# Optimization experiments

Measured on AMD Instinct MI355X. Metric: run time of the kernel, lower is better.

Reference implementation:

```python
import jax, jax.numpy as jnp
import numpy as np

N = 100_000   # num nodes
E = 1_600_000 # num edges (before self-loops)
IN = 128      # in_channels (FEATURE_DIM)
H = 64        # hidden_channels (HIDDEN_DIM)
NEG_SLOPE = 0.2


def setup_inputs() -> dict:
    key = jax.random.key(0)
    ks = jax.random.split(key, 8)
    s = 0.05
    return {
        "x": jax.random.normal(ks[0], (N, IN), jnp.float32),
        "edge_index": jax.random.randint(ks[1], (2, E), 0, N, jnp.int32),
        "W_gat": jax.random.normal(ks[2], (IN, H), jnp.float32) * s,
        "att_src": jax.random.normal(ks[3], (H,), jnp.float32) * s,
        "att_dst": jax.random.normal(ks[4], (H,), jnp.float32) * s,
        "b_gat": jnp.zeros((H,), jnp.float32),
        "W1": jax.random.normal(ks[5], (H, H), jnp.float32) * s,
        "b1": jnp.zeros((H,), jnp.float32),
        "W2": jax.random.normal(ks[6], (H, H), jnp.float32) * s,
        "b2": jnp.zeros((H,), jnp.float32),
    }


def _add_self_loops(src, dst, n):
    loop = jnp.arange(n, dtype=src.dtype)
    return jnp.concatenate([src, loop]), jnp.concatenate([dst, loop])


def _segment_softmax(e, seg, n):
    # numerically stable softmax over edges grouped by target node
    m = jax.ops.segment_max(e, seg, num_segments=n)
    m = jnp.where(jnp.isfinite(m), m, 0.0)  # empty segments
    ex = jnp.exp(e - m[seg])
    s = jax.ops.segment_sum(ex, seg, num_segments=n)
    return ex / (s[seg] + 1e-16)


def gat_conv(x, W, a_src, a_dst, b, src, dst, n):
    # PyG GATConv, heads=1: h = xW; e_ij = LeakyReLU(a_s.h_j + a_d.h_i)
    h = x @ W                                   # [N,H]
    alpha_s = h @ a_src                         # [N]
    alpha_d = h @ a_dst                         # [N]
    e = jax.nn.leaky_relu(alpha_s[src] + alpha_d[dst], NEG_SLOPE)  # [E]
    alpha = _segment_softmax(e, dst, n)         # [E]
    out = jax.ops.segment_sum(alpha[:, None] * h[src], dst, num_segments=n)
    return out + b


def gcn_conv(x, W, b, src, dst, n):
    # PyG GCNConv: symmetric normalization D^-1/2 A D^-1/2 (self-loops already added)
    h = x @ W                                   # [N,H]
    deg = jax.ops.segment_sum(jnp.ones(src.shape, h.dtype), dst, num_segments=n)
    dinv = jnp.where(deg > 0, jax.lax.rsqrt(deg), 0.0)
    norm = dinv[src] * dinv[dst]                # [E]
    out = jax.ops.segment_sum(norm[:, None] * h[src], dst, num_segments=n)
    return out + b


def reference(x, edge_index, W_gat, att_src, att_dst, b_gat, W1, b1, W2, b2):
    n = x.shape[0]
    src, dst = _add_self_loops(edge_index[0], edge_index[1], n)
    h = jax.nn.relu(gat_conv(x, W_gat, att_src, att_dst, b_gat, src, dst, n))
    h = jax.nn.relu(gcn_conv(h, W1, b1, src, dst, n))
    h = gcn_conv(h, W2, b2, src, dst, n)
    return h
```

## Files before the change

### kernel.cpp

```cpp
#include <hip/hip_runtime.h>
#include <hip/hip_bf16.h>
#include <math.h>

#define IN_CH 128
#define H_CH  64
#define PBLK  256
#define PTHR  512
#define BKT   256
#define MAXBK 400


__device__ inline float bflo(unsigned u) { return __uint_as_float(u << 16); }
__device__ inline float bfhi(unsigned u) { return __uint_as_float(u & 0xffff0000u); }
__device__ inline unsigned short f2bf(float f) {
    unsigned x = __float_as_uint(f);
    return (unsigned short)((x + 0x7fffu + ((x >> 16) & 1u)) >> 16);
}


__global__ __launch_bounds__(PTHR) void passA(const int* __restrict__ ei, int E, int n,
                                              int nbk, int* __restrict__ blkhist) {
    __shared__ int hist[MAXBK];
    int tot = E + n;
    int CH = (tot + gridDim.x - 1) / gridDim.x;
    int beg = blockIdx.x * CH, end = min(tot, beg + CH);
    for (int k = threadIdx.x; k < nbk; k += blockDim.x) hist[k] = 0;
    __syncthreads();
    for (int idx = beg + threadIdx.x; idx < end; idx += blockDim.x) {
        int d = (idx < E) ? ei[E + idx] : (idx - E);
        atomicAdd(&hist[d >> 8], 1);
    }
    __syncthreads();
    for (int k = threadIdx.x; k < nbk; k += blockDim.x)
        blkhist[(size_t)blockIdx.x * nbk + k] = hist[k];
}

__global__ __launch_bounds__(PBLK) void passB1(const int* __restrict__ blkhist,
                                               int* __restrict__ blkbase,
                                               int* __restrict__ btot, int nbk) {
    __shared__ int sh[PBLK];
    int k = blockIdx.x, t = threadIdx.x;
    int v = blkhist[(size_t)t * nbk + k];
    sh[t] = v;
    __syncthreads();
    for (int off = 1; off < PBLK; off <<= 1) {
        int x = (t >= off) ? sh[t - off] : 0;
        __syncthreads();
        sh[t] += x;
        __syncthreads();
    }
    blkbase[(size_t)t * nbk + k] = sh[t] - v;
    if (t == PBLK - 1) btot[k] = sh[PBLK - 1];
}

__global__ __launch_bounds__(512) void passB2(const int* __restrict__ btot,
                                              int* __restrict__ bbase, int nbk, int tot) {
    __shared__ int sh[512];
    int t = threadIdx.x;
    int v = (t < nbk) ? btot[t] : 0;
    sh[t] = v;
    __syncthreads();
    for (int off = 1; off < 512; off <<= 1) {
        int x = (t >= off) ? sh[t - off] : 0;
        __syncthreads();
        sh[t] += x;
        __syncthreads();
    }
    if (t < nbk) bbase[t] = sh[t] - v;
    if (t == 0) bbase[nbk] = tot;
}

__global__ __launch_bounds__(PTHR) void passC(const int* __restrict__ ei, int E, int n, int nbk,
                                              const int* __restrict__ bbase,
                                              const int* __restrict__ blkbase,
                                              int2* __restrict__ pairs) {
    __shared__ int cur[MAXBK];
    int tot = E + n;
    int CH = (tot + gridDim.x - 1) / gridDim.x;
    int beg = blockIdx.x * CH, end = min(tot, beg + CH);
    for (int k = threadIdx.x; k < nbk; k += blockDim.x)
        cur[k] = bbase[k] + blkbase[(size_t)blockIdx.x * nbk + k];
    __syncthreads();
    for (int idx = beg + threadIdx.x; idx < end; idx += blockDim.x) {
        int s, d;
        if (idx < E) { s = ei[idx]; d = ei[E + idx]; }
        else         { s = idx - E; d = idx - E; }
        int pos = atomicAdd(&cur[d >> 8], 1);
        pairs[pos] = make_int2(s, d);
    }
}

__global__ __launch_bounds__(BKT) void passD(const int2* __restrict__ pairs,
                                             const int* __restrict__ bbase, int n, int nbk, int EP,
                                             int* __restrict__ esrc, int* __restrict__ offsets,
                                             float* __restrict__ dinv) {
    __shared__ int cnt[BKT];
    __shared__ int sh[BKT];
    __shared__ int cur[BKT];
    int k = blockIdx.x;
    int nbeg = k << 8;
    int t = threadIdx.x;
    int ebeg = bbase[k], eend = bbase[k + 1];
    cnt[t] = 0;
    __syncthreads();
    for (int e = ebeg + t; e < eend; e += BKT) {
        int2 p = pairs[e];
        atomicAdd(&cnt[p.y - nbeg], 1);
    }
    __syncthreads();
    int v = cnt[t];
    sh[t] = v;
    __syncthreads();
    for (int off = 1; off < BKT; off <<= 1) {
        int x = (t >= off) ? sh[t - off] : 0;
        __syncthreads();
        sh[t] += x;
        __syncthreads();
    }
    int lp = sh[t] - v;
    cur[t] = lp;
    int gn = nbeg + t;
    if (gn < n) {
        offsets[gn] = ebeg + lp;
        dinv[gn] = rsqrtf((float)v);
    }
    __syncthreads();
    for (int e = ebeg + t; e < eend; e += BKT) {
        int2 p = pairs[e];
        int pos = ebeg + atomicAdd(&cur[p.y - nbeg], 1);
        esrc[pos] = p.x;
    }
    if (k == 0 && t == 0) offsets[n] = EP;
}


template <int K, bool GAT, bool OUTBF, bool BIASF>
__global__ __launch_bounds__(512, 6) void gemm_tiled(const float* __restrict__ X,
                                                     const float* __restrict__ W,
                                                     void* __restrict__ outv,
                                                     const float* __restrict__ asw,
                                                     const float* __restrict__ adw,
                                                     float* __restrict__ alpha_s,
                                                     float* __restrict__ alpha_d,
                                                     const float* __restrict__ bias, int n) {
    __shared__ float Wl[K][68];
    int t  = threadIdx.x;
    int tx = t & 15, ty = t >> 4;
    int r0 = blockIdx.x * 128;

#pragma unroll
    for (int i = 0; i < K / 32; i++) {
        int f = t + 512 * i;
        int k = f >> 4, cq = (f & 15) << 2;
        float4 v = *(const float4*)(W + k * H_CH + cq);
        *(float4*)&Wl[k][cq] = v;
    }
    __syncthreads();

    const float* xp[4];
#pragma unroll
    for (int j = 0; j < 4; j++) {
        int r = r0 + 4 * ty + j;
        xp[j] = X + (size_t)(r < n ? r : 0) * K;
    }

    float acc[4][4] = {};
#pragma unroll 4
    for (int k4 = 0; k4 < K; k4 += 4) {
        float4 xr[4], wr[4];
#pragma unroll
        for (int j = 0; j < 4; j++)  xr[j]  = *(const float4*)(xp[j] + k4);
#pragma unroll
        for (int kk = 0; kk < 4; kk++) wr[kk] = *(const float4*)&Wl[k4 + kk][4 * tx];
#pragma unroll
        for (int j = 0; j < 4; j++) {
            acc[j][0] += xr[j].x * wr[0].x; acc[j][1] += xr[j].x * wr[0].y;
            acc[j][2] += xr[j].x * wr[0].z; acc[j][3] += xr[j].x * wr[0].w;
            acc[j][0] += xr[j].y * wr[1].x; acc[j][1] += xr[j].y * wr[1].y;
            acc[j][2] += xr[j].y * wr[1].z; acc[j][3] += xr[j].y * wr[1].w;
            acc[j][0] += xr[j].z * wr[2].x; acc[j][1] += xr[j].z * wr[2].y;
            acc[j][2] += xr[j].z * wr[2].z; acc[j][3] += xr[j].z * wr[2].w;
            acc[j][0] += xr[j].w * wr[3].x; acc[j][1] += xr[j].w * wr[3].y;
            acc[j][2] += xr[j].w * wr[3].z; acc[j][3] += xr[j].w * wr[3].w;
        }
    }

    float4 bvv = make_float4(0.f, 0.f, 0.f, 0.f);
    if (BIASF) bvv = *(const float4*)(bias + 4 * tx);

#pragma unroll
    for (int j = 0; j < 4; j++) {
        int r = r0 + 4 * ty + j;
        if (r < n) {
            float o0 = acc[j][0] + bvv.x, o1 = acc[j][1] + bvv.y;
            float o2 = acc[j][2] + bvv.z, o3 = acc[j][3] + bvv.w;
            if (OUTBF) {
                ushort4 o;
                o.x = f2bf(o0); o.y = f2bf(o1); o.z = f2bf(o2); o.w = f2bf(o3);
                *(ushort4*)((unsigned short*)outv + (size_t)r * H_CH + 4 * tx) = o;
            } else {
                *(float4*)((float*)outv + (size_t)r * H_CH + 4 * tx) =
                    make_float4(o0, o1, o2, o3);
            }
        }
    }

    if (GAT) {
        float va0 = asw[4 * tx], va1 = asw[4 * tx + 1], va2 = asw[4 * tx + 2], va3 = asw[4 * tx + 3];
        float vd0 = adw[4 * tx], vd1 = adw[4 * tx + 1], vd2 = adw[4 * tx + 2], vd3 = adw[4 * tx + 3];
#pragma unroll
        for (int j = 0; j < 4; j++) {
            float s1 = acc[j][0] * va0 + acc[j][1] * va1 + acc[j][2] * va2 + acc[j][3] * va3;
            float s2 = acc[j][0] * vd0 + acc[j][1] * vd1 + acc[j][2] * vd2 + acc[j][3] * vd3;
#pragma unroll
            for (int off = 8; off; off >>= 1) {
                s1 += __shfl_xor(s1, off, 16);
                s2 += __shfl_xor(s2, off, 16);
            }
            int r = r0 + 4 * ty + j;
            if (tx == 0 && r < n) { alpha_s[r] = s1; alpha_d[r] = s2; }
        }
    }
}


__global__ __launch_bounds__(256) void gat_gather(const unsigned short* __restrict__ h,
                                                  const int* __restrict__ offs,
                                                  const int* __restrict__ esrc,
                                                  const float* __restrict__ as,
                                                  const float* __restrict__ ad,
                                                  const float* __restrict__ bias,
                                                  float* __restrict__ out, int n) {
    __shared__ int2 sh[4][64];
    int lane = threadIdx.x & 63;
    int wid  = threadIdx.x >> 6;
    int q = lane >> 4, c = lane & 15;
    int gw = (blockIdx.x * blockDim.x + threadIdx.x) >> 6;
    int nw = (gridDim.x * blockDim.x) >> 6;
    float4 bv = *(const float4*)(bias + 4 * c);
    for (int i = gw; i < n; i += nw) {
        int beg = offs[i], end = offs[i + 1];
        float adi = ad[i];
        float a0 = 0.f, a1 = 0.f, a2 = 0.f, a3 = 0.f, s = 0.f;
        for (int base = beg; base < end; base += 64) {
            int l = base + lane;
            int sj = 0; float p = 0.f;
            if (l < end) {
                sj = esrc[l];
                float a = as[sj] + adi;
                float ev = a > 0.f ? a : 0.2f * a;
                p = __expf(ev);
            }
            sh[wid][lane] = make_int2(sj, __float_as_int(p));
            int cnt = min(64, end - base);
            int k = 0;
            for (; k + 8 <= cnt; k += 8) {
                int2 tA = sh[wid][k + q];
                int2 tB = sh[wid][k + 4 + q];
                float pA = __int_as_float(tA.y);
                float pB = __int_as_float(tB.y);
                uint2 uA = *(const uint2*)(h + (size_t)tA.x * H_CH + 4 * c);
                uint2 uB = *(const uint2*)(h + (size_t)tB.x * H_CH + 4 * c);
                a0 += pA * bflo(uA.x); a1 += pA * bfhi(uA.x);
                a2 += pA * bflo(uA.y); a3 += pA * bfhi(uA.y);
                a0 += pB * bflo(uB.x); a1 += pB * bfhi(uB.x);
                a2 += pB * bflo(uB.y); a3 += pB * bfhi(uB.y);
                s += pA + pB;
            }
            for (; k < cnt; k += 4) {
                int2 tA = sh[wid][k + q];
                float pA = __int_as_float(tA.y);
                uint2 uA = *(const uint2*)(h + (size_t)tA.x * H_CH + 4 * c);
                a0 += pA * bflo(uA.x); a1 += pA * bfhi(uA.x);
                a2 += pA * bflo(uA.y); a3 += pA * bfhi(uA.y);
                s += pA;
            }
        }
        a0 += __shfl_xor(a0, 16, 64); a0 += __shfl_xor(a0, 32, 64);
        a1 += __shfl_xor(a1, 16, 64); a1 += __shfl_xor(a1, 32, 64);
        a2 += __shfl_xor(a2, 16, 64); a2 += __shfl_xor(a2, 32, 64);
        a3 += __shfl_xor(a3, 16, 64); a3 += __shfl_xor(a3, 32, 64);
        s  += __shfl_xor(s, 16, 64);  s  += __shfl_xor(s, 32, 64);
        float invs = 1.f / (s + 1e-16f);
        if (q == 0) {
            float4 o;
            o.x = fmaxf(a0 * invs + bv.x, 0.f);
            o.y = fmaxf(a1 * invs + bv.y, 0.f);
            o.z = fmaxf(a2 * invs + bv.z, 0.f);
            o.w = fmaxf(a3 * invs + bv.w, 0.f);
            *(float4*)(out + (size_t)i * H_CH + 4 * c) = o;
        }
    }
}


template <bool OUTBF, bool RELU, bool BIASF>
__global__ __launch_bounds__(256) void gcn_gather(const unsigned short* __restrict__ h,
                                                  const int* __restrict__ offs,
                                                  const int* __restrict__ esrc,
                                                  const float* __restrict__ dinv,
                                                  const float* __restrict__ bias,
                                                  void* __restrict__ outv, int n) {
    __shared__ int2 sh[4][64];
    int lane = threadIdx.x & 63;
    int wid  = threadIdx.x >> 6;
    int q = lane >> 4, c = lane & 15;
    int gw = (blockIdx.x * blockDim.x + threadIdx.x) >> 6;
    int nw = (gridDim.x * blockDim.x) >> 6;
    float4 bv = make_float4(0.f, 0.f, 0.f, 0.f);
    if (BIASF) bv = *(const float4*)(bias + 4 * c);
    for (int i = gw; i < n; i += nw) {
        int beg = offs[i], end = offs[i + 1];
        float a0 = 0.f, a1 = 0.f, a2 = 0.f, a3 = 0.f;
        for (int base = beg; base < end; base += 64) {
            int l = base + lane;
            int sj = 0; float wl = 0.f;
            if (l < end) { sj = esrc[l]; wl = dinv[sj]; }
            sh[wid][lane] = make_int2(sj, __float_as_int(wl));
            int cnt = min(64, end - base);
            int k = 0;
            for (; k + 8 <= cnt; k += 8) {
                int2 tA = sh[wid][k + q];
                int2 tB = sh[wid][k + 4 + q];
                float pA = __int_as_float(tA.y);
                float pB = __int_as_float(tB.y);
                uint2 uA = *(const uint2*)(h + (size_t)tA.x * H_CH + 4 * c);
                uint2 uB = *(const uint2*)(h + (size_t)tB.x * H_CH + 4 * c);
                a0 += pA * bflo(uA.x); a1 += pA * bfhi(uA.x);
                a2 += pA * bflo(uA.y); a3 += pA * bfhi(uA.y);
                a0 += pB * bflo(uB.x); a1 += pB * bfhi(uB.x);
                a2 += pB * bflo(uB.y); a3 += pB * bfhi(uB.y);
            }
            for (; k < cnt; k += 4) {
                int2 tA = sh[wid][k + q];
                float pA = __int_as_float(tA.y);
                uint2 uA = *(const uint2*)(h + (size_t)tA.x * H_CH + 4 * c);
                a0 += pA * bflo(uA.x); a1 += pA * bfhi(uA.x);
                a2 += pA * bflo(uA.y); a3 += pA * bfhi(uA.y);
            }
        }
        a0 += __shfl_xor(a0, 16, 64); a0 += __shfl_xor(a0, 32, 64);
        a1 += __shfl_xor(a1, 16, 64); a1 += __shfl_xor(a1, 32, 64);
        a2 += __shfl_xor(a2, 16, 64); a2 += __shfl_xor(a2, 32, 64);
        a3 += __shfl_xor(a3, 16, 64); a3 += __shfl_xor(a3, 32, 64);
        float di = dinv[i];
        if (q == 0) {
            float v0 = a0 * di + bv.x, v1 = a1 * di + bv.y;
            float v2 = a2 * di + bv.z, v3 = a3 * di + bv.w;
            if (RELU) {
                v0 = fmaxf(v0, 0.f); v1 = fmaxf(v1, 0.f);
                v2 = fmaxf(v2, 0.f); v3 = fmaxf(v3, 0.f);
            }
            if (OUTBF) {
                ushort4 o;
                o.x = f2bf(v0); o.y = f2bf(v1); o.z = f2bf(v2); o.w = f2bf(v3);
                *(ushort4*)((unsigned short*)outv + (size_t)i * H_CH + 4 * c) = o;
            } else {
                *(float4*)((float*)outv + (size_t)i * H_CH + 4 * c) =
                    make_float4(v0, v1, v2, v3);
            }
        }
    }
}


extern "C" void kernel_launch(void* const* d_in, const int* in_sizes, int n_in,
                              void* d_out, int out_size, void* d_ws, size_t ws_size,
                              hipStream_t stream) {
    const float* x       = (const float*)d_in[0];
    const int*   ei      = (const int*)d_in[1];
    const float* W_gat   = (const float*)d_in[2];
    const float* att_src = (const float*)d_in[3];
    const float* att_dst = (const float*)d_in[4];
    const float* b_gat   = (const float*)d_in[5];
    const float* W1      = (const float*)d_in[6];
    const float* b1      = (const float*)d_in[7];
    const float* W2      = (const float*)d_in[8];
    const float* b2      = (const float*)d_in[9];
    float* out = (float*)d_out;

    const int N  = in_sizes[0] / IN_CH;
    const int E  = in_sizes[1] / 2;
    const int EP = E + N;
    const int NBK = (N + BKT - 1) / BKT;
    const int NT  = (N + 127) / 128;

    char* p = (char*)d_ws;
    auto alloc = [&](size_t bytes) -> void* {
        void* r = (void*)p;
        p += (bytes + 255) & ~(size_t)255;
        return r;
    };
    float* bufA    = (float*)alloc((size_t)N * H_CH * 4);
    unsigned short* hbf  = (unsigned short*)alloc((size_t)N * H_CH * 2);
    unsigned short* hbf2 = (unsigned short*)alloc((size_t)N * H_CH * 2);
    float* alpha_s = (float*)alloc((size_t)N * 4);
    float* alpha_d = (float*)alloc((size_t)N * 4);
    float* dinv    = (float*)alloc((size_t)N * 4);
    int*   offsets = (int*)alloc((size_t)(N + 1) * 4);
    int*   esrc    = (int*)alloc((size_t)EP * 4);
    int2*  pairs   = (int2*)alloc((size_t)EP * 8);
    int*   blkhist = (int*)alloc((size_t)PBLK * NBK * 4);
    int*   blkbase = (int*)alloc((size_t)PBLK * NBK * 4);
    int*   btot    = (int*)alloc((size_t)(NBK + 1) * 4);
    int*   bbase   = (int*)alloc((size_t)(NBK + 1) * 4);

    passA<<<PBLK, PTHR, 0, stream>>>(ei, E, N, NBK, blkhist);
    passB1<<<NBK, PBLK, 0, stream>>>(blkhist, blkbase, btot, NBK);
    passB2<<<1, 512, 0, stream>>>(btot, bbase, NBK, EP);
    passC<<<PBLK, PTHR, 0, stream>>>(ei, E, N, NBK, bbase, blkbase, pairs);
    passD<<<NBK, BKT, 0, stream>>>(pairs, bbase, N, NBK, EP, esrc, offsets, dinv);

    gemm_tiled<IN_CH, true, true, false><<<NT, 512, 0, stream>>>(x, W_gat, hbf, att_src, att_dst,
                                                                 alpha_s, alpha_d, nullptr, N);
    gat_gather<<<2048, 256, 0, stream>>>(hbf, offsets, esrc, alpha_s, alpha_d, b_gat, bufA, N);

    gemm_tiled<H_CH, false, true, false><<<NT, 512, 0, stream>>>(bufA, W1, hbf, nullptr, nullptr,
                                                                 nullptr, nullptr, nullptr, N);
    gcn_gather<true, true, true><<<2048, 256, 0, stream>>>(hbf, offsets, esrc, dinv, b1, hbf2, N);

    gcn_gather<false, false, false><<<2048, 256, 0, stream>>>(hbf2, offsets, esrc, dinv, nullptr,
                                                              bufA, N);
    gemm_tiled<H_CH, false, false, true><<<NT, 512, 0, stream>>>(bufA, W2, out, nullptr, nullptr,
                                                                 nullptr, nullptr, b2, N);
}
```

Before: 251.3 us.

## Replace FP32 tiled GEMMs with bf16 MFMA GEMM and fold attention into weights

The three dense projections now run as a wave-level bf16 MFMA kernel (16x16x32) with W fragments kept in registers, instead of an FP32 FMA tile kernel. GAT attention logits are computed straight from x using the precomputed vectors W·att_src and W·att_dst, which a small prep kernel produces. This is meant to cut GEMM compute time, but the inputs are rounded to bf16 before the MFMA and outputs are written with scalar, less coalesced stores. The GEMMs are a minor part of a pipeline that is dominated by the gathers.

```diff
diff --git a/kernel.cpp b/kernel.cpp
--- a/kernel.cpp
+++ b/kernel.cpp
@@ -9,12 +9,25 @@
 #define BKT   256
 #define MAXBK 400
 
+typedef __attribute__((ext_vector_type(8))) short bf16x8;
+typedef __attribute__((ext_vector_type(4))) float f32x4;
+
 
 __device__ inline float bflo(unsigned u) { return __uint_as_float(u << 16); }
 __device__ inline float bfhi(unsigned u) { return __uint_as_float(u & 0xffff0000u); }
 __device__ inline unsigned short f2bf(float f) {
     unsigned x = __float_as_uint(f);
     return (unsigned short)((x + 0x7fffu + ((x >> 16) & 1u)) >> 16);
+}
+__device__ inline bf16x8 pack8(float4 lo, float4 hi) {
+    union { bf16x8 v; unsigned short u[8]; } r;
+    r.u[0] = f2bf(lo.x); r.u[1] = f2bf(lo.y); r.u[2] = f2bf(lo.z); r.u[3] = f2bf(lo.w);
+    r.u[4] = f2bf(hi.x); r.u[5] = f2bf(hi.y); r.u[6] = f2bf(hi.z); r.u[7] = f2bf(hi.w);
+    return r.v;
+}
+__device__ inline float dot8(float4 a0, float4 a1, float4 b0, float4 b1) {
+    return a0.x * b0.x + a0.y * b0.y + a0.z * b0.z + a0.w * b0.w
+         + a1.x * b1.x + a1.y * b1.y + a1.z * b1.z + a1.w * b1.w;
 }
 
 
@@ -134,91 +147,108 @@
 }
 
 
+__global__ void wprep(const float* __restrict__ W, const float* __restrict__ as,
+                      const float* __restrict__ ad, float* __restrict__ w_as,
+                      float* __restrict__ w_ad, int K) {
+    int k = blockIdx.x * blockDim.x + threadIdx.x;
+    if (k < K) {
+        float s = 0.f, d = 0.f;
+        for (int c = 0; c < H_CH; c++) {
+            float w = W[(size_t)k * H_CH + c];
+            s += w * as[c];
+            d += w * ad[c];
+        }
+        w_as[k] = s;
+        w_ad[k] = d;
+    }
+}
+
+
 template <int K, bool GAT, bool OUTBF, bool BIASF>
-__global__ __launch_bounds__(512, 6) void gemm_tiled(const float* __restrict__ X,
-                                                     const float* __restrict__ W,
-                                                     void* __restrict__ outv,
-                                                     const float* __restrict__ asw,
-                                                     const float* __restrict__ adw,
-                                                     float* __restrict__ alpha_s,
-                                                     float* __restrict__ alpha_d,
-                                                     const float* __restrict__ bias, int n) {
-    __shared__ float Wl[K][68];
-    int t  = threadIdx.x;
-    int tx = t & 15, ty = t >> 4;
-    int r0 = blockIdx.x * 128;
-
-#pragma unroll
-    for (int i = 0; i < K / 32; i++) {
-        int f = t + 512 * i;
-        int k = f >> 4, cq = (f & 15) << 2;
-        float4 v = *(const float4*)(W + k * H_CH + cq);
-        *(float4*)&Wl[k][cq] = v;
-    }
-    __syncthreads();
-
-    const float* xp[4];
-#pragma unroll
-    for (int j = 0; j < 4; j++) {
-        int r = r0 + 4 * ty + j;
-        xp[j] = X + (size_t)(r < n ? r : 0) * K;
-    }
-
-    float acc[4][4] = {};
-#pragma unroll 4
-    for (int k4 = 0; k4 < K; k4 += 4) {
-        float4 xr[4], wr[4];
-#pragma unroll
-        for (int j = 0; j < 4; j++)  xr[j]  = *(const float4*)(xp[j] + k4);
-#pragma unroll
-        for (int kk = 0; kk < 4; kk++) wr[kk] = *(const float4*)&Wl[k4 + kk][4 * tx];
-#pragma unroll
-        for (int j = 0; j < 4; j++) {
-            acc[j][0] += xr[j].x * wr[0].x; acc[j][1] += xr[j].x * wr[0].y;
-            acc[j][2] += xr[j].x * wr[0].z; acc[j][3] += xr[j].x * wr[0].w;
-            acc[j][0] += xr[j].y * wr[1].x; acc[j][1] += xr[j].y * wr[1].y;
-            acc[j][2] += xr[j].y * wr[1].z; acc[j][3] += xr[j].y * wr[1].w;
-            acc[j][0] += xr[j].z * wr[2].x; acc[j][1] += xr[j].z * wr[2].y;
-            acc[j][2] += xr[j].z * wr[2].z; acc[j][3] += xr[j].z * wr[2].w;
-            acc[j][0] += xr[j].w * wr[3].x; acc[j][1] += xr[j].w * wr[3].y;
-            acc[j][2] += xr[j].w * wr[3].z; acc[j][3] += xr[j].w * wr[3].w;
-        }
-    }
-
-    float4 bvv = make_float4(0.f, 0.f, 0.f, 0.f);
-    if (BIASF) bvv = *(const float4*)(bias + 4 * tx);
-
-#pragma unroll
-    for (int j = 0; j < 4; j++) {
-        int r = r0 + 4 * ty + j;
-        if (r < n) {
-            float o0 = acc[j][0] + bvv.x, o1 = acc[j][1] + bvv.y;
-            float o2 = acc[j][2] + bvv.z, o3 = acc[j][3] + bvv.w;
-            if (OUTBF) {
-                ushort4 o;
-                o.x = f2bf(o0); o.y = f2bf(o1); o.z = f2bf(o2); o.w = f2bf(o3);
-                *(ushort4*)((unsigned short*)outv + (size_t)r * H_CH + 4 * tx) = o;
-            } else {
-                *(float4*)((float*)outv + (size_t)r * H_CH + 4 * tx) =
-                    make_float4(o0, o1, o2, o3);
-            }
-        }
-    }
-
-    if (GAT) {
-        float va0 = asw[4 * tx], va1 = asw[4 * tx + 1], va2 = asw[4 * tx + 2], va3 = asw[4 * tx + 3];
-        float vd0 = adw[4 * tx], vd1 = adw[4 * tx + 1], vd2 = adw[4 * tx + 2], vd3 = adw[4 * tx + 3];
-#pragma unroll
-        for (int j = 0; j < 4; j++) {
-            float s1 = acc[j][0] * va0 + acc[j][1] * va1 + acc[j][2] * va2 + acc[j][3] * va3;
-            float s2 = acc[j][0] * vd0 + acc[j][1] * vd1 + acc[j][2] * vd2 + acc[j][3] * vd3;
-#pragma unroll
-            for (int off = 8; off; off >>= 1) {
-                s1 += __shfl_xor(s1, off, 16);
-                s2 += __shfl_xor(s2, off, 16);
-            }
-            int r = r0 + 4 * ty + j;
-            if (tx == 0 && r < n) { alpha_s[r] = s1; alpha_d[r] = s2; }
+__global__ __launch_bounds__(256) void mfma_gemm(const float* __restrict__ X,
+                                                 const float* __restrict__ W,
+                                                 void* __restrict__ outv,
+                                                 const float* __restrict__ w_as,
+                                                 const float* __restrict__ w_ad,
+                                                 float* __restrict__ alpha_s,
+                                                 float* __restrict__ alpha_d,
+                                                 const float* __restrict__ bias, int n) {
+    constexpr int KF = K / 32;
+    int lane = threadIdx.x & 63;
+    int wid  = threadIdx.x >> 6;
+    int col  = lane & 15;
+    int grp  = lane >> 4;
+
+    bf16x8 bfr[KF][4];
+#pragma unroll
+    for (int kf = 0; kf < KF; kf++) {
+        int kb = 32 * kf + 8 * grp;
+#pragma unroll
+        for (int cf = 0; cf < 4; cf++) {
+            float w0[8];
+#pragma unroll
+            for (int e = 0; e < 8; e++)
+                w0[e] = W[(size_t)(kb + e) * H_CH + 16 * cf + col];
+            bfr[kf][cf] = pack8(make_float4(w0[0], w0[1], w0[2], w0[3]),
+                                make_float4(w0[4], w0[5], w0[6], w0[7]));
+        }
+    }
+    float bb[4] = {0.f, 0.f, 0.f, 0.f};
+    if (BIASF) {
+#pragma unroll
+        for (int cf = 0; cf < 4; cf++) bb[cf] = bias[16 * cf + col];
+    }
+
+    int gw = blockIdx.x * (blockDim.x >> 6) + wid;
+    int nw = gridDim.x * (blockDim.x >> 6);
+    int ns = (n + 15) >> 4;
+    for (int s = gw; s < ns; s += nw) {
+        int r0 = s << 4;
+        int r  = r0 + col;
+        const float* xr = X + (size_t)(r < n ? r : 0) * K;
+        bf16x8 afr[KF];
+        float ps = 0.f, pd = 0.f;
+#pragma unroll
+        for (int kf = 0; kf < KF; kf++) {
+            int kb = 32 * kf + 8 * grp;
+            float4 x0 = *(const float4*)(xr + kb);
+            float4 x1 = *(const float4*)(xr + kb + 4);
+            if (GAT) {
+                float4 s0 = *(const float4*)(w_as + kb);
+                float4 s1 = *(const float4*)(w_as + kb + 4);
+                float4 d0 = *(const float4*)(w_ad + kb);
+                float4 d1 = *(const float4*)(w_ad + kb + 4);
+                ps += dot8(x0, x1, s0, s1);
+                pd += dot8(x0, x1, d0, d1);
+            }
+            afr[kf] = pack8(x0, x1);
+        }
+        f32x4 acc[4];
+#pragma unroll
+        for (int cf = 0; cf < 4; cf++) {
+            acc[cf] = (f32x4){0.f, 0.f, 0.f, 0.f};
+#pragma unroll
+            for (int kf = 0; kf < KF; kf++)
+                acc[cf] = __builtin_amdgcn_mfma_f32_16x16x32_bf16(afr[kf], bfr[kf][cf],
+                                                                  acc[cf], 0, 0, 0);
+        }
+#pragma unroll
+        for (int cf = 0; cf < 4; cf++) {
+            int cc = 16 * cf + col;
+#pragma unroll
+            for (int g = 0; g < 4; g++) {
+                int rr = r0 + 4 * grp + g;
+                if (rr < n) {
+                    float v = acc[cf][g] + bb[cf];
+                    if (OUTBF) ((unsigned short*)outv)[(size_t)rr * H_CH + cc] = f2bf(v);
+                    else       ((float*)outv)[(size_t)rr * H_CH + cc] = v;
+                }
+            }
+        }
+        if (GAT) {
+            ps += __shfl_xor(ps, 16, 64); ps += __shfl_xor(ps, 32, 64);
+            pd += __shfl_xor(pd, 16, 64); pd += __shfl_xor(pd, 32, 64);
+            if (grp == 0 && r < n) { alpha_s[r] = ps; alpha_d[r] = pd; }
         }
     }
 }
@@ -383,7 +413,6 @@
     const int E  = in_sizes[1] / 2;
     const int EP = E + N;
     const int NBK = (N + BKT - 1) / BKT;
-    const int NT  = (N + 127) / 128;
 
     char* p = (char*)d_ws;
     auto alloc = [&](size_t bytes) -> void* {
@@ -397,6 +426,8 @@
     float* alpha_s = (float*)alloc((size_t)N * 4);
     float* alpha_d = (float*)alloc((size_t)N * 4);
     float* dinv    = (float*)alloc((size_t)N * 4);
+    float* w_as_g  = (float*)alloc((size_t)IN_CH * 4);
+    float* w_ad_g  = (float*)alloc((size_t)IN_CH * 4);
     int*   offsets = (int*)alloc((size_t)(N + 1) * 4);
     int*   esrc    = (int*)alloc((size_t)EP * 4);
     int2*  pairs   = (int2*)alloc((size_t)EP * 8);
@@ -405,22 +436,24 @@
     int*   btot    = (int*)alloc((size_t)(NBK + 1) * 4);
     int*   bbase   = (int*)alloc((size_t)(NBK + 1) * 4);
 
+    wprep<<<1, 128, 0, stream>>>(W_gat, att_src, att_dst, w_as_g, w_ad_g, IN_CH);
+
     passA<<<PBLK, PTHR, 0, stream>>>(ei, E, N, NBK, blkhist);
     passB1<<<NBK, PBLK, 0, stream>>>(blkhist, blkbase, btot, NBK);
     passB2<<<1, 512, 0, stream>>>(btot, bbase, NBK, EP);
     passC<<<PBLK, PTHR, 0, stream>>>(ei, E, N, NBK, bbase, blkbase, pairs);
     passD<<<NBK, BKT, 0, stream>>>(pairs, bbase, N, NBK, EP, esrc, offsets, dinv);
 
-    gemm_tiled<IN_CH, true, true, false><<<NT, 512, 0, stream>>>(x, W_gat, hbf, att_src, att_dst,
+    mfma_gemm<IN_CH, true, true, false><<<512, 256, 0, stream>>>(x, W_gat, hbf, w_as_g, w_ad_g,
                                                                  alpha_s, alpha_d, nullptr, N);
     gat_gather<<<2048, 256, 0, stream>>>(hbf, offsets, esrc, alpha_s, alpha_d, b_gat, bufA, N);
 
-    gemm_tiled<H_CH, false, true, false><<<NT, 512, 0, stream>>>(bufA, W1, hbf, nullptr, nullptr,
+    mfma_gemm<H_CH, false, true, false><<<512, 256, 0, stream>>>(bufA, W1, hbf, nullptr, nullptr,
                                                                  nullptr, nullptr, nullptr, N);
     gcn_gather<true, true, true><<<2048, 256, 0, stream>>>(hbf, offsets, esrc, dinv, b1, hbf2, N);
 
     gcn_gather<false, false, false><<<2048, 256, 0, stream>>>(hbf2, offsets, esrc, dinv, nullptr,
                                                               bufA, N);
-    gemm_tiled<H_CH, false, false, true><<<NT, 512, 0, stream>>>(bufA, W2, out, nullptr, nullptr,
+    mfma_gemm<H_CH, false, false, true><<<512, 256, 0, stream>>>(bufA, W2, out, nullptr, nullptr,
                                                                  nullptr, nullptr, b2, N);
 }
```

Result: faster. 207.3 us (-17.5%).
